# Kernel optimization log

Measured on AMD Instinct MI355X. Metric: run time of the kernel, lower is better.

Reference implementation:

```python
import jax, jax.numpy as jnp
import numpy as np

NEG_INF = -9e15
ALPHA = 0.2  # LeakyReLU negative slope

N = 8192
D_IN = 512
D_OUT = 256


def setup_inputs() -> dict:
    key = jax.random.key(0)
    k1, k2, k3, k4, k5 = jax.random.split(key, 5)
    features = jax.random.normal(k1, (N, D_IN), dtype=jnp.float32)
    adjacency_matrix = jax.random.randint(k2, (N, N), 0, 2, dtype=jnp.int32)
    # learned params (torch Linear stores [out, in]; we use [in, out] layout)
    s_phi = 1.0 / np.sqrt(D_IN)
    W_phi = jax.random.uniform(k3, (D_IN, D_OUT), jnp.float32, -s_phi, s_phi)
    s_v = 1.0 / np.sqrt(D_OUT)
    w_mu = jax.random.uniform(k4, (D_OUT,), jnp.float32, -s_v, s_v)
    w_xi = jax.random.uniform(k5, (D_OUT,), jnp.float32, -s_v, s_v)
    return {"features": features, "adjacency_matrix": adjacency_matrix,
            "W_phi": W_phi, "w_mu": w_mu, "w_xi": w_xi}


def reference(features, adjacency_matrix, W_phi, w_mu, w_xi):
    h = features @ W_phi                                   # [N, d_out]
    mu = h @ w_mu                                          # [N]
    xi = h @ w_xi                                          # [N]
    e = mu[:, None] + xi[None, :]                          # [N, N] additive scores
    e = jnp.where(e >= 0, e, ALPHA * e)                    # LeakyReLU
    e = jnp.where(adjacency_matrix > 0, e, NEG_INF)        # mask non-edges
    a = jax.nn.softmax(e, axis=1)                          # row softmax (dropout p=0)
    out = a @ h                                            # weighted aggregation
    return jax.nn.elu(out)
```

## Files before the change

### kernel.cpp

```cpp
#include <hip/hip_runtime.h>
#include <cstdint>
#include <cstddef>


#define LOG2E 1.44269504f

typedef __attribute__((ext_vector_type(8))) short short8;
typedef __attribute__((ext_vector_type(4))) float floatx4;

using uint_as1 = __attribute__((address_space(1))) unsigned int;
using uint_as3 = __attribute__((address_space(3))) unsigned int;

__device__ __forceinline__ void gld_lds16(const void* g, void* l) {
  __builtin_amdgcn_global_load_lds((const uint_as1*)g, (uint_as3*)l, 16, 0, 0);
}

__device__ __forceinline__ unsigned short f2b(float f) {
  unsigned u = __float_as_uint(f);
  u += 0x7fffu + ((u >> 16) & 1u);
  return (unsigned short)(u >> 16);
}
__device__ __forceinline__ float b2f(short s) {
  return __uint_as_float(((unsigned)(unsigned short)s) << 16);
}

__global__ void k_bitmaskz(const int* __restrict__ adj,
                           const float* __restrict__ Emu, const float* __restrict__ Fmu,
                           const float* __restrict__ Exi, const float* __restrict__ Fxi,
                           unsigned long long* __restrict__ bm, float* __restrict__ zbuf) {
  int gw = (blockIdx.x * 256 + threadIdx.x) >> 6;
  int lane = threadIdx.x & 63;
  float EM = Emu[gw], FM = Fmu[gw];
  size_t w0 = (size_t)gw * 128;
  float z = 0.f;
  for (int r = 0; r < 128; r += 4) {
    size_t wd = w0 + r;
    int v0 = adj[(wd + 0) * 64 + lane];
    int v1 = adj[(wd + 1) * 64 + lane];
    int v2 = adj[(wd + 2) * 64 + lane];
    int v3 = adj[(wd + 3) * 64 + lane];
    float e0 = Exi[(r + 0) * 64 + lane], f0 = Fxi[(r + 0) * 64 + lane];
    float e1 = Exi[(r + 1) * 64 + lane], f1 = Fxi[(r + 1) * 64 + lane];
    float e2 = Exi[(r + 2) * 64 + lane], f2 = Fxi[(r + 2) * 64 + lane];
    float e3 = Exi[(r + 3) * 64 + lane], f3 = Fxi[(r + 3) * 64 + lane];
    unsigned long long m0 = __ballot(v0 != 0);
    unsigned long long m1 = __ballot(v1 != 0);
    unsigned long long m2 = __ballot(v2 != 0);
    unsigned long long m3 = __ballot(v3 != 0);
    z += (v0 != 0) ? fmaxf(EM * e0, FM * f0) : 0.f;
    z += (v1 != 0) ? fmaxf(EM * e1, FM * f1) : 0.f;
    z += (v2 != 0) ? fmaxf(EM * e2, FM * f2) : 0.f;
    z += (v3 != 0) ? fmaxf(EM * e3, FM * f3) : 0.f;
    if (lane == 0) {
      bm[wd] = m0; bm[wd + 1] = m1; bm[wd + 2] = m2; bm[wd + 3] = m3;
    }
  }
#pragma unroll
  for (int off = 32; off > 0; off >>= 1) z += __shfl_xor(z, off);
  if (lane == 0) zbuf[gw] = z;
}

__global__ void k_cvt_features(const float* __restrict__ f, unsigned short* __restrict__ fb) {
  int tid = blockIdx.x * 256 + threadIdx.x;
  float4 v = ((const float4*)f)[tid];
  ushort4 o = {f2b(v.x), f2b(v.y), f2b(v.z), f2b(v.w)};
  *(ushort4*)&fb[tid * 4] = o;
}

__global__ void k_prep_wt(const float* __restrict__ w, unsigned short* __restrict__ wt) {
  int tid = blockIdx.x * 256 + threadIdx.x;
  int n = tid >> 9, k = tid & 511;
  wt[n * 512 + k] = f2b(w[k * 256 + n]);
}

__global__ void k_prep_p(const float* __restrict__ w, const float* __restrict__ wmu,
                         const float* __restrict__ wxi, float* __restrict__ pmu,
                         float* __restrict__ pxi) {
  int tid = blockIdx.x * 256 + threadIdx.x;
  int k = tid >> 2, seg = tid & 3;
  float sm = 0.f, sx = 0.f;
  int base = k * 256 + seg * 64;
#pragma unroll
  for (int c = 0; c < 64; c += 4) {
    float4 wv = *(const float4*)&w[base + c];
    float4 mv = *(const float4*)&wmu[seg * 64 + c];
    float4 xv = *(const float4*)&wxi[seg * 64 + c];
    sm += wv.x * mv.x + wv.y * mv.y + wv.z * mv.z + wv.w * mv.w;
    sx += wv.x * xv.x + wv.y * xv.y + wv.z * xv.z + wv.w * xv.w;
  }
  sm += __shfl_xor(sm, 1); sm += __shfl_xor(sm, 2);
  sx += __shfl_xor(sx, 1); sx += __shfl_xor(sx, 2);
  if (seg == 0) { pmu[k] = sm; pxi[k] = sx; }
}

__global__ void k_mu_xi(const unsigned short* __restrict__ fb, const float* __restrict__ pmu,
                        const float* __restrict__ pxi, float* __restrict__ Emu,
                        float* __restrict__ Fmu, float* __restrict__ Exi,
                        float* __restrict__ Fxi) {
  int w = threadIdx.x >> 6, l = threadIdx.x & 63;
  int i = blockIdx.x * 4 + w;
  short8 fv = *(const short8*)&fb[i * 512 + l * 8];
  float m = 0.f, x = 0.f;
#pragma unroll
  for (int c = 0; c < 8; ++c) {
    float fvf = b2f(fv[c]);
    m = fmaf(fvf, pmu[l * 8 + c], m);
    x = fmaf(fvf, pxi[l * 8 + c], x);
  }
#pragma unroll
  for (int off = 32; off > 0; off >>= 1) {
    m += __shfl_xor(m, off);
    x += __shfl_xor(x, off);
  }
  if (l == 0) {
    float ms = m * LOG2E, xs = x * LOG2E;
    Emu[i] = __builtin_amdgcn_exp2f(ms);
    Fmu[i] = __builtin_amdgcn_exp2f(0.2f * ms);
    Exi[i] = __builtin_amdgcn_exp2f(xs);
    Fxi[i] = __builtin_amdgcn_exp2f(0.2f * xs);
  }
}

__global__ __launch_bounds__(256, 2) void k_gemm1(const unsigned short* __restrict__ fb,
                                                  const unsigned short* __restrict__ wt,
                                                  unsigned short* __restrict__ ht) {
  __shared__ __align__(16) unsigned short As[64 * 64];
  __shared__ __align__(16) unsigned short Bs[128 * 64];
  int t = threadIdx.x, w = t >> 6, l = t & 63;
  int bm_ = blockIdx.x >> 1, bn = blockIdx.x & 1;
  int m0 = bm_ * 64, n0 = bn * 128;
  int lr = l >> 3, lg = l & 7, g = lg ^ lr;
  int kg = l >> 4, ln = l & 15;
  floatx4 zero = {0.f, 0.f, 0.f, 0.f};
  floatx4 acc[4][2];
#pragma unroll
  for (int mf = 0; mf < 4; ++mf)
#pragma unroll
    for (int nf = 0; nf < 2; ++nf) acc[mf][nf] = zero;

  for (int it = 0; it < 8; ++it) {
    int k0 = it * 64;
#pragma unroll
    for (int q = 0; q < 2; ++q) {
      int row = w * 16 + q * 8 + lr;
      const void* gp = fb + (size_t)(m0 + row) * 512 + k0 + g * 8;
      int lb = __builtin_amdgcn_readfirstlane((w * 16 + q * 8) * 64);
      gld_lds16(gp, &As[lb]);
    }
#pragma unroll
    for (int q = 0; q < 4; ++q) {
      int row = w * 32 + q * 8 + lr;
      const void* gp = wt + (size_t)(n0 + row) * 512 + k0 + g * 8;
      int lb = __builtin_amdgcn_readfirstlane((w * 32 + q * 8) * 64);
      gld_lds16(gp, &Bs[lb]);
    }
    __syncthreads();
#pragma unroll
    for (int ks = 0; ks < 2; ++ks) {
      int gg = ks * 4 + kg;
      int swz = (gg ^ (ln & 7)) * 8;
      short8 bfr[2];
#pragma unroll
      for (int nf = 0; nf < 2; ++nf)
        bfr[nf] = *(const short8*)&Bs[(w * 32 + nf * 16 + ln) * 64 + swz];
#pragma unroll
      for (int mf = 0; mf < 4; ++mf) {
        short8 afr = *(const short8*)&As[(mf * 16 + ln) * 64 + swz];
#pragma unroll
        for (int nf = 0; nf < 2; ++nf)
          acc[mf][nf] = __builtin_amdgcn_mfma_f32_16x16x32_bf16(afr, bfr[nf], acc[mf][nf], 0, 0, 0);
      }
    }
    __syncthreads();
  }
#pragma unroll
  for (int mf = 0; mf < 4; ++mf)
#pragma unroll
    for (int nf = 0; nf < 2; ++nf) {
      int ng = n0 + w * 32 + nf * 16 + ln;
      int mg = m0 + mf * 16 + kg * 4;
      ushort4 o = {f2b(acc[mf][nf][0]), f2b(acc[mf][nf][1]),
                   f2b(acc[mf][nf][2]), f2b(acc[mf][nf][3])};
      *(ushort4*)&ht[(size_t)ng * 8192 + mg] = o;
    }
}

__global__ __launch_bounds__(512, 2) void k_gatt3(const unsigned char* __restrict__ bm8,
                                                  const unsigned short* __restrict__ ht,
                                                  const float* __restrict__ Emu,
                                                  const float* __restrict__ Fmu,
                                                  const float* __restrict__ Exi,
                                                  const float* __restrict__ Fxi,
                                                  float* __restrict__ nump) {
  __shared__ __align__(16) unsigned short Bs[2][256 * 128];
  __shared__ __align__(16) unsigned char BitS[2][128 * 16];
  __shared__ __align__(16) float EfE[2048];
  __shared__ __align__(16) float EfF[2048];

  int t = threadIdx.x, w = t >> 6, l = t & 63;
  int ln = l & 15, kg = l >> 4;
  int wi = w >> 1, wn = w & 1;
  int jb = blockIdx.x & 3, ig = blockIdx.x >> 2;
  int i0 = ig * 128;
  int jc0 = jb * 2048;

  {
    float4 e = *(const float4*)&Exi[jc0 + t * 4];
    float4 f = *(const float4*)&Fxi[jc0 + t * 4];
    *(float4*)&EfE[t * 4] = e;
    *(float4*)&EfF[t * 4] = f;
  }

  float EM[2], FM[2];
#pragma unroll
  for (int mf = 0; mf < 2; ++mf) {
    int i = i0 + wi * 32 + mf * 16 + ln;
    EM[mf] = Emu[i];
    FM[mf] = Fmu[i];
  }

  floatx4 zero = {0.f, 0.f, 0.f, 0.f};
  floatx4 acc[2][8];
#pragma unroll
  for (int mf = 0; mf < 2; ++mf)
#pragma unroll
    for (int nf = 0; nf < 8; ++nf) acc[mf][nf] = zero;

#define STAGE_HW(hw_, nb_)                                                    \
  {                                                                           \
    int j0_ = jc0 + (hw_) * 128;                                              \
    _Pragma("unroll")                                                         \
    for (int q = 0; q < 8; ++q) {                                             \
      int r0 = w * 32 + q * 4;                                                \
      int row = r0 + (l >> 4);                                                \
      int g = (l & 15) ^ (row & 15);                                          \
      const void* gp = ht + (size_t)row * 8192 + j0_ + g * 8;                 \
      int lb = __builtin_amdgcn_readfirstlane(r0 * 128);                      \
      gld_lds16(gp, &Bs[nb_][lb]);                                            \
    }                                                                         \
    if (w < 2) {                                                              \
      int row = w * 64 + l;                                                   \
      const void* gp = bm8 + (size_t)(i0 + row) * 1024 + (j0_ >> 3);          \
      int lb = __builtin_amdgcn_readfirstlane(w * 64 * 16);                   \
      gld_lds16(gp, &BitS[nb_][lb]);                                          \
    }                                                                         \
  }

  STAGE_HW(0, 0);
  __syncthreads();

  for (int hw = 0; hw < 16; ++hw) {
    int nb = hw & 1;
    if (hw < 15) STAGE_HW(hw + 1, nb ^ 1);
#pragma unroll
    for (int ksl = 0; ksl < 4; ++ksl) {
      int gran = ksl * 4 + kg;
      int jl = hw * 128 + gran * 8;
      float4 e0 = *(const float4*)&EfE[jl];
      float4 e1 = *(const float4*)&EfE[jl + 4];
      float4 f0 = *(const float4*)&EfF[jl];
      float4 f1 = *(const float4*)&EfF[jl + 4];
      float ex[8] = {e0.x, e0.y, e0.z, e0.w, e1.x, e1.y, e1.z, e1.w};
      float fx[8] = {f0.x, f0.y, f0.z, f0.w, f1.x, f1.y, f1.z, f1.w};
      short8 bfv[8];
#pragma unroll
      for (int nf = 0; nf < 8; ++nf) {
        int n = wn * 128 + nf * 16 + ln;
        bfv[nf] = *(const short8*)&Bs[nb][n * 128 + ((gran ^ (n & 15)) * 8)];
      }
#pragma unroll
      for (int mf = 0; mf < 2; ++mf) {
        int row = wi * 32 + mf * 16 + ln;
        unsigned bw = *(const unsigned*)&BitS[nb][row * 16 + ksl * 4];
        unsigned bits = (bw >> (kg * 8)) & 0xffu;
        float A = EM[mf], F = FM[mf];
        short8 af;
#pragma unroll
        for (int e = 0; e < 8; ++e) {
          float m = fmaxf(A * ex[e], F * fx[e]);
          m = (bits & (1u << e)) ? m : 0.f;
          af[e] = (short)f2b(m);
        }
#pragma unroll
        for (int nf = 0; nf < 8; ++nf)
          acc[mf][nf] = __builtin_amdgcn_mfma_f32_16x16x32_bf16(af, bfv[nf], acc[mf][nf], 0, 0, 0);
      }
    }
    __syncthreads();
  }

  float* np = nump + (size_t)jb * (8192 * 256);
#pragma unroll
  for (int mf = 0; mf < 2; ++mf) {
    int rowb = i0 + wi * 32 + mf * 16 + kg * 4;
#pragma unroll
    for (int r = 0; r < 4; ++r) {
      float* rp = np + (size_t)(rowb + r) * 256 + wn * 128;
#pragma unroll
      for (int nf = 0; nf < 8; ++nf)
        rp[nf * 16 + ln] = acc[mf][nf][r];
    }
  }
#undef STAGE_HW
}

__global__ void k_final(const float* __restrict__ nump, const float* __restrict__ zbuf,
                        float* __restrict__ out) {
  int tid = blockIdx.x * 256 + threadIdx.x;
  int i = tid >> 6;
  float zi = 1.0f / zbuf[i];
  float4 v = {0.f, 0.f, 0.f, 0.f};
#pragma unroll
  for (int p = 0; p < 4; ++p) {
    float4 s = *(const float4*)&nump[(size_t)p * (8192 * 256) + tid * 4];
    v.x += s.x; v.y += s.y; v.z += s.z; v.w += s.w;
  }
  v.x *= zi; v.y *= zi; v.z *= zi; v.w *= zi;
  v.x = (v.x > 0.f) ? v.x : (__builtin_amdgcn_exp2f(v.x * LOG2E) - 1.f);
  v.y = (v.y > 0.f) ? v.y : (__builtin_amdgcn_exp2f(v.y * LOG2E) - 1.f);
  v.z = (v.z > 0.f) ? v.z : (__builtin_amdgcn_exp2f(v.z * LOG2E) - 1.f);
  v.w = (v.w > 0.f) ? v.w : (__builtin_amdgcn_exp2f(v.w * LOG2E) - 1.f);
  *(float4*)&out[tid * 4] = v;
}

extern "C" void kernel_launch(void* const* d_in, const int* in_sizes, int n_in,
                              void* d_out, int out_size, void* d_ws, size_t ws_size,
                              hipStream_t stream) {
  const float* features = (const float*)d_in[0];
  const int* adjm = (const int*)d_in[1];
  const float* W_phi = (const float*)d_in[2];
  const float* w_mu = (const float*)d_in[3];
  const float* w_xi = (const float*)d_in[4];
  float* out = (float*)d_out;

  char* ws = (char*)d_ws;
  unsigned short* fb  = (unsigned short*)(ws + 0);
  unsigned short* ht  = (unsigned short*)(ws + 8388608);
  unsigned short* wt  = (unsigned short*)(ws + 12582912);
  float* pmu = (float*)(ws + 12845056);
  float* pxi = (float*)(ws + 12847104);
  float* Emu = (float*)(ws + 12849152);
  float* Fmu = (float*)(ws + 12881920);
  float* Exi = (float*)(ws + 12914688);
  float* Fxi = (float*)(ws + 12947456);
  float* zbuf = (float*)(ws + 12980224);
  unsigned char* bmask = (unsigned char*)(ws + 13631488);
  float* nump = (float*)(ws + 25165824);

  k_cvt_features<<<4096, 256, 0, stream>>>(features, fb);
  k_prep_wt<<<512, 256, 0, stream>>>(W_phi, wt);
  k_prep_p<<<8, 256, 0, stream>>>(W_phi, w_mu, w_xi, pmu, pxi);
  k_mu_xi<<<2048, 256, 0, stream>>>(fb, pmu, pxi, Emu, Fmu, Exi, Fxi);
  k_gemm1<<<256, 256, 0, stream>>>(fb, wt, ht);
  k_bitmaskz<<<2048, 256, 0, stream>>>(adjm, Emu, Fmu, Exi, Fxi,
                                       (unsigned long long*)bmask, zbuf);
  k_gatt3<<<256, 512, 0, stream>>>(bmask, ht, Emu, Fmu, Exi, Fxi, nump);
  k_final<<<2048, 256, 0, stream>>>(nump, zbuf, out);
}
```

Baseline: 472.6 us.

## Retile attention GEMM to full-width waves with 8-way split-K and resident bitmask

```diff
diff --git a/kernel.cpp b/kernel.cpp
--- a/kernel.cpp
+++ b/kernel.cpp
@@ -185,123 +185,138 @@
     }
 }
 
-__global__ __launch_bounds__(512, 2) void k_gatt3(const unsigned char* __restrict__ bm8,
+__global__ __launch_bounds__(512, 2) void k_gatt5(const unsigned char* __restrict__ bm8,
                                                   const unsigned short* __restrict__ ht,
                                                   const float* __restrict__ Emu,
                                                   const float* __restrict__ Fmu,
                                                   const float* __restrict__ Exi,
                                                   const float* __restrict__ Fxi,
                                                   float* __restrict__ nump) {
-  __shared__ __align__(16) unsigned short Bs[2][256 * 128];
-  __shared__ __align__(16) unsigned char BitS[2][128 * 16];
-  __shared__ __align__(16) float EfE[2048];
-  __shared__ __align__(16) float EfF[2048];
+  __shared__ __align__(16) unsigned short Bs[2][256 * 64];
+  __shared__ __align__(16) unsigned char BitAll[256 * 128];
+  __shared__ __align__(16) float EfE[1024];
+  __shared__ __align__(16) float EfF[1024];
 
   int t = threadIdx.x, w = t >> 6, l = t & 63;
   int ln = l & 15, kg = l >> 4;
-  int wi = w >> 1, wn = w & 1;
-  int jb = blockIdx.x & 3, ig = blockIdx.x >> 2;
-  int i0 = ig * 128;
-  int jc0 = jb * 2048;
-
-  {
-    float4 e = *(const float4*)&Exi[jc0 + t * 4];
-    float4 f = *(const float4*)&Fxi[jc0 + t * 4];
-    *(float4*)&EfE[t * 4] = e;
-    *(float4*)&EfF[t * 4] = f;
+  int jb = blockIdx.x & 7, ig = blockIdx.x >> 3;
+  int i0 = ig * 256;
+  int jc0 = jb * 1024;
+
+  if (t < 256) {
+    *(float4*)&EfE[t * 4] = *(const float4*)&Exi[jc0 + t * 4];
+  } else {
+    int t2 = t - 256;
+    *(float4*)&EfF[t2 * 4] = *(const float4*)&Fxi[jc0 + t2 * 4];
+  }
+#pragma unroll
+  for (int r = 0; r < 4; ++r) {
+    int c = r * 512 + t;
+    int row = c >> 3, gp_ = c & 7;
+    int g = gp_ ^ (row & 7);
+    const void* src = bm8 + (size_t)(i0 + row) * 1024 + jb * 128 + g * 16;
+    int lb = __builtin_amdgcn_readfirstlane((r * 512 + w * 64) * 16);
+    gld_lds16(src, &BitAll[lb]);
   }
 
   float EM[2], FM[2];
 #pragma unroll
   for (int mf = 0; mf < 2; ++mf) {
-    int i = i0 + wi * 32 + mf * 16 + ln;
+    int i = i0 + w * 32 + mf * 16 + ln;
     EM[mf] = Emu[i];
     FM[mf] = Fmu[i];
   }
 
   floatx4 zero = {0.f, 0.f, 0.f, 0.f};
-  floatx4 acc[2][8];
+  floatx4 acc[2][16];
 #pragma unroll
   for (int mf = 0; mf < 2; ++mf)
 #pragma unroll
-    for (int nf = 0; nf < 8; ++nf) acc[mf][nf] = zero;
-
-#define STAGE_HW(hw_, nb_)                                                    \
+    for (int nf = 0; nf < 16; ++nf) acc[mf][nf] = zero;
+
+#define STAGE(hw_, b_)                                                        \
   {                                                                           \
-    int j0_ = jc0 + (hw_) * 128;                                              \
+    int j0_ = jc0 + (hw_) * 64;                                               \
     _Pragma("unroll")                                                         \
-    for (int q = 0; q < 8; ++q) {                                             \
-      int r0 = w * 32 + q * 4;                                                \
-      int row = r0 + (l >> 4);                                                \
-      int g = (l & 15) ^ (row & 15);                                          \
+    for (int q = 0; q < 4; ++q) {                                             \
+      int r0 = w * 32 + q * 8;                                                \
+      int row = r0 + (l >> 3);                                                \
+      int g = (l & 7) ^ (row & 7);                                            \
       const void* gp = ht + (size_t)row * 8192 + j0_ + g * 8;                 \
-      int lb = __builtin_amdgcn_readfirstlane(r0 * 128);                      \
-      gld_lds16(gp, &Bs[nb_][lb]);                                            \
+      int lb = __builtin_amdgcn_readfirstlane((b_) * (256 * 64) + r0 * 64);   \
+      gld_lds16(gp, &Bs[0][lb]);                                              \
     }                                                                         \
-    if (w < 2) {                                                              \
-      int row = w * 64 + l;                                                   \
-      const void* gp = bm8 + (size_t)(i0 + row) * 1024 + (j0_ >> 3);          \
-      int lb = __builtin_amdgcn_readfirstlane(w * 64 * 16);                   \
-      gld_lds16(gp, &BitS[nb_][lb]);                                          \
-    }                                                                         \
-  }
-
-  STAGE_HW(0, 0);
+  }
+
+  STAGE(0, 0);
   __syncthreads();
 
   for (int hw = 0; hw < 16; ++hw) {
-    int nb = hw & 1;
-    if (hw < 15) STAGE_HW(hw + 1, nb ^ 1);
-#pragma unroll
-    for (int ksl = 0; ksl < 4; ++ksl) {
+    int buf = hw & 1;
+    if (hw < 15) STAGE(hw + 1, buf ^ 1);
+
+    unsigned long long bw[2];
+#pragma unroll
+    for (int mf = 0; mf < 2; ++mf) {
+      int rowL = w * 32 + mf * 16 + ln;
+      bw[mf] = *(const unsigned long long*)
+          &BitAll[rowL * 128 + (((hw >> 1) ^ (rowL & 7)) * 16) + (hw & 1) * 8];
+    }
+
+#pragma unroll
+    for (int ksl = 0; ksl < 2; ++ksl) {
       int gran = ksl * 4 + kg;
-      int jl = hw * 128 + gran * 8;
+      int jl = hw * 64 + gran * 8;
       float4 e0 = *(const float4*)&EfE[jl];
       float4 e1 = *(const float4*)&EfE[jl + 4];
       float4 f0 = *(const float4*)&EfF[jl];
       float4 f1 = *(const float4*)&EfF[jl + 4];
       float ex[8] = {e0.x, e0.y, e0.z, e0.w, e1.x, e1.y, e1.z, e1.w};
       float fx[8] = {f0.x, f0.y, f0.z, f0.w, f1.x, f1.y, f1.z, f1.w};
-      short8 bfv[8];
-#pragma unroll
-      for (int nf = 0; nf < 8; ++nf) {
-        int n = wn * 128 + nf * 16 + ln;
-        bfv[nf] = *(const short8*)&Bs[nb][n * 128 + ((gran ^ (n & 15)) * 8)];
-      }
+      short8 af[2];
 #pragma unroll
       for (int mf = 0; mf < 2; ++mf) {
-        int row = wi * 32 + mf * 16 + ln;
-        unsigned bw = *(const unsigned*)&BitS[nb][row * 16 + ksl * 4];
-        unsigned bits = (bw >> (kg * 8)) & 0xffu;
+        unsigned bits = (unsigned)(bw[mf] >> ((ksl * 4 + kg) * 8)) & 0xffu;
         float A = EM[mf], F = FM[mf];
-        short8 af;
 #pragma unroll
         for (int e = 0; e < 8; ++e) {
           float m = fmaxf(A * ex[e], F * fx[e]);
           m = (bits & (1u << e)) ? m : 0.f;
-          af[e] = (short)f2b(m);
+          af[mf][e] = (short)f2b(m);
         }
-#pragma unroll
-        for (int nf = 0; nf < 8; ++nf)
-          acc[mf][nf] = __builtin_amdgcn_mfma_f32_16x16x32_bf16(af, bfv[nf], acc[mf][nf], 0, 0, 0);
       }
+#pragma unroll
+      for (int half = 0; half < 2; ++half) {
+        short8 bfv[8];
+#pragma unroll
+        for (int nf = 0; nf < 8; ++nf) {
+          int n = half * 128 + nf * 16 + ln;
+          bfv[nf] = *(const short8*)&Bs[buf][n * 64 + ((gran ^ (n & 7)) * 8)];
+        }
+#pragma unroll
+        for (int mf = 0; mf < 2; ++mf)
+#pragma unroll
+          for (int nf = 0; nf < 8; ++nf)
+            acc[mf][half * 8 + nf] = __builtin_amdgcn_mfma_f32_16x16x32_bf16(
+                af[mf], bfv[nf], acc[mf][half * 8 + nf], 0, 0, 0);
+      }
     }
     __syncthreads();
   }
+#undef STAGE
 
   float* np = nump + (size_t)jb * (8192 * 256);
 #pragma unroll
   for (int mf = 0; mf < 2; ++mf) {
-    int rowb = i0 + wi * 32 + mf * 16 + kg * 4;
+    int rowb = i0 + w * 32 + mf * 16 + kg * 4;
 #pragma unroll
     for (int r = 0; r < 4; ++r) {
-      float* rp = np + (size_t)(rowb + r) * 256 + wn * 128;
-#pragma unroll
-      for (int nf = 0; nf < 8; ++nf)
+      float* rp = np + (size_t)(rowb + r) * 256;
+#pragma unroll
+      for (int nf = 0; nf < 16; ++nf)
         rp[nf * 16 + ln] = acc[mf][nf][r];
     }
   }
-#undef STAGE_HW
 }
 
 __global__ void k_final(const float* __restrict__ nump, const float* __restrict__ zbuf,
@@ -311,7 +326,7 @@
   float zi = 1.0f / zbuf[i];
   float4 v = {0.f, 0.f, 0.f, 0.f};
 #pragma unroll
-  for (int p = 0; p < 4; ++p) {
+  for (int p = 0; p < 8; ++p) {
     float4 s = *(const float4*)&nump[(size_t)p * (8192 * 256) + tid * 4];
     v.x += s.x; v.y += s.y; v.z += s.z; v.w += s.w;
   }
@@ -354,6 +369,6 @@
   k_gemm1<<<256, 256, 0, stream>>>(fb, wt, ht);
   k_bitmaskz<<<2048, 256, 0, stream>>>(adjm, Emu, Fmu, Exi, Fxi,
                                        (unsigned long long*)bmask, zbuf);
-  k_gatt3<<<256, 512, 0, stream>>>(bmask, ht, Emu, Fmu, Exi, Fxi, nump);
+  k_gatt5<<<256, 512, 0, stream>>>(bmask, ht, Emu, Fmu, Exi, Fxi, nump);
   k_final<<<2048, 256, 0, stream>>>(nump, zbuf, out);
 }
```

New measurement: 471.0 us. About the same (-0.3%).
